# Kernel optimization log

Hardware: AMD Instinct MI355X
Metric: run time of the kernel (lower is better)

Reference implementation:

```python
import jax, jax.numpy as jnp
import numpy as np

N_NODES = 50000
N_REL = 3
N_EDGES = 500000
D_IN, D_HID, D_OUT = 128, 256, 128


def setup_inputs() -> dict:
    key = jax.random.key(0)
    ks = jax.random.split(key, 9)
    def w(k, shape, fan_in):
        return jax.random.normal(k, shape, dtype=jnp.float32) / np.sqrt(fan_in)
    return {
        "x": jax.random.normal(ks[0], (N_NODES, D_IN), dtype=jnp.float32),
        "src": jax.random.randint(ks[1], (N_REL, N_EDGES), 0, N_NODES, dtype=jnp.int32),
        "dst": jax.random.randint(ks[2], (N_REL, N_EDGES), 0, N_NODES, dtype=jnp.int32),
        "w_self1": w(ks[3], (N_REL, D_IN, D_HID), D_IN),
        "w_neigh1": w(ks[4], (N_REL, D_IN, D_HID), D_IN),
        "b1": jnp.zeros((N_REL, D_HID), dtype=jnp.float32),
        "w_self2": w(ks[5], (N_REL, D_HID, D_OUT), D_HID),
        "w_neigh2": w(ks[6], (N_REL, D_HID, D_OUT), D_HID),
        "b2": jnp.zeros((N_REL, D_OUT), dtype=jnp.float32),
    }


def _sage_hetero_layer(x, src, dst, w_self, w_neigh, b):
    """Multi-relation SAGEConv (mean agg); relation outputs summed (HeteroGraphConv default).
    x: [N, din]; src/dst: [R, E]; w_*: [R, din, dout]; b: [R, dout]."""
    n = x.shape[0]

    def per_rel(s, d, ws, wn, bb):
        gathered = jnp.take(x, s, axis=0)                      # [E, din] neighbor gather
        summed = jax.ops.segment_sum(gathered, d, num_segments=n)  # [N, din]
        deg = jax.ops.segment_sum(jnp.ones(s.shape, jnp.float32), d, num_segments=n)
        h_neigh = summed / jnp.maximum(deg, 1.0)[:, None]      # mean, 0 for isolated dst
        return x @ ws + h_neigh @ wn + bb                      # fc_self + fc_neigh + bias

    per_rel_out = jax.vmap(per_rel)(src, dst, w_self, w_neigh, b)  # [R, N, dout]
    return per_rel_out.sum(axis=0)


def reference(x, src, dst, w_self1, w_neigh1, b1, w_self2, w_neigh2, b2):
    h = _sage_hetero_layer(x, src, dst, w_self1, w_neigh1, b1)
    h = jax.nn.relu(h)  # SAGEConv activation in hidden layers
    out = _sage_hetero_layer(h, src, dst, w_self2, w_neigh2, b2)  # last layer: no activation
    return out
```

## Files before the change

kernel.cpp:

```cpp
#include <hip/hip_runtime.h>

#define NN 50000
#define NREL 3
#define NE 500000
#define DIN 128
#define DHID 256
#define DOUT 128

#define NBUK 98
#define CAP 8192
#define EPB 2048
#define NCHK ((NE + EPB - 1) / EPB)
#define PA_BLKS (NREL * NCHK)
#define F2B_BLKS 6250
#define ZROW ((uint)NN << 8)

typedef unsigned int uint;
typedef unsigned short ushort;
typedef __attribute__((ext_vector_type(8))) short bf16x8;
typedef __attribute__((ext_vector_type(4))) float f32x4;

using gptr_t = const __attribute__((address_space(1))) unsigned int*;
using lptr_t = __attribute__((address_space(3))) unsigned int*;

__device__ __forceinline__ ushort f2bf(float f) {
    uint u = __float_as_uint(f);
    uint r = (u + 0x7fffu + ((u >> 16) & 1u)) >> 16;
    return (ushort)r;
}
__device__ __forceinline__ void acc2(float2& a, uint u) {
    a.x += __uint_as_float(u << 16);
    a.y += __uint_as_float(u & 0xffff0000u);
}

__global__ __launch_bounds__(256) void pass_a_prep(
    const int* __restrict__ src, const int* __restrict__ dst,
    int* __restrict__ bcursor, uint* __restrict__ pairs,
    const float* __restrict__ x, ushort* __restrict__ xb,
    const float* __restrict__ ws1, const float* __restrict__ wn1, ushort* __restrict__ Bt1,
    const float* __restrict__ ws2, const float* __restrict__ wn2, ushort* __restrict__ Bt2,
    const float* __restrict__ b1, float* __restrict__ bsum1,
    const float* __restrict__ b2, float* __restrict__ bsum2,
    ushort* __restrict__ agg0, ushort* __restrict__ agg1, ushort* __restrict__ agg2) {
    int blk = blockIdx.x, tid = threadIdx.x;
    if (blk < PA_BLKS) {
        int r = blk / NCHK;
        int chunk = blk % NCHK;
        int e0 = chunk * EPB;
        int nedge = min(EPB, NE - e0);
        const int* S = src + (size_t)r * NE + e0;
        const int* D = dst + (size_t)r * NE + e0;
        __shared__ int cnt[NBUK], base[NBUK], cur[NBUK];
        if (tid < NBUK) { cnt[tid] = 0; cur[tid] = 0; }
        __syncthreads();
        uint pk[8];
        int bk[8];
        bool val[8];
#pragma unroll
        for (int j = 0; j < 8; ++j) {
            int e = j * 256 + tid;
            val[j] = e < nedge;
            int d = val[j] ? D[e] : 0;
            int s = val[j] ? S[e] : 0;
            bk[j] = d >> 9;
            pk[j] = ((uint)s << 9) | (uint)(d & 511);
            if (val[j]) atomicAdd(&cnt[bk[j]], 1);
        }
        __syncthreads();
        if (tid < NBUK) base[tid] = atomicAdd(&bcursor[r * NBUK + tid], cnt[tid]);
        __syncthreads();
#pragma unroll
        for (int j = 0; j < 8; ++j) {
            if (val[j]) {
                int slot = base[bk[j]] + atomicAdd(&cur[bk[j]], 1);
                if (slot < CAP) pairs[(size_t)(r * NBUK + bk[j]) * CAP + slot] = pk[j];
            }
        }
        return;
    }
    blk -= PA_BLKS;
    if (blk < F2B_BLKS) {
        int t = blk * 256 + tid;
        float4 v = *(const float4*)(x + (size_t)t * 4);
        uint2 p;
        p.x = (uint)f2bf(v.x) | ((uint)f2bf(v.y) << 16);
        p.y = (uint)f2bf(v.z) | ((uint)f2bf(v.w) << 16);
        *(uint2*)(xb + (size_t)t * 4) = p;
    } else if (blk < F2B_BLKS + 512) {
        int t = (blk - F2B_BLKS) * 256 + tid;
        int n = t >> 9, k = t & 511;
        int b = k >> 7, kk = k & 127;
        float v;
        if (b == 0)
            v = ws1[kk * 256 + n] + ws1[128 * 256 + kk * 256 + n] + ws1[2 * 128 * 256 + kk * 256 + n];
        else
            v = wn1[(size_t)(b - 1) * 128 * 256 + kk * 256 + n];
        Bt1[t] = f2bf(v);
    } else if (blk < F2B_BLKS + 1024) {
        int t = (blk - F2B_BLKS - 512) * 256 + tid;
        int n = t >> 8, k = t & 255;
        int c = n >> 7, j = n & 127;
        float v;
        if (c == 0)
            v = ws2[k * 128 + j] + ws2[256 * 128 + k * 128 + j] + ws2[2 * 256 * 128 + k * 128 + j];
        else
            v = wn2[(size_t)(c - 1) * 256 * 128 + k * 128 + j];
        Bt2[t] = f2bf(v);
    } else {
        if (tid < DHID) bsum1[tid] = b1[tid] + b1[DHID + tid] + b1[2 * DHID + tid];
        if (tid < DOUT) bsum2[tid] = b2[tid] + b2[DOUT + tid] + b2[2 * DOUT + tid];
        if (tid >= 192 && tid < 256) {
            int b = (tid - 192) >> 4, i = tid & 15;
            ushort* row = (b == 0) ? xb : (b == 1) ? agg0 : (b == 2) ? agg1 : agg2;
            uint4 z = {0u, 0u, 0u, 0u};
            *(uint4*)(row + (size_t)NN * 128 + i * 8) = z;
        }
    }
}

__global__ __launch_bounds__(256) void pass_b(const uint* __restrict__ pairs,
                                              const int* __restrict__ bcnt,
                                              uint* __restrict__ srclist,
                                              int* __restrict__ deg,
                                              int* __restrict__ offs) {
    int blk = blockIdx.x;
    int b = blk % NBUK;
    int r = blk / NBUK;
    int node_base = b * 512;
    int count = min(bcnt[blk], CAP);
    int obase = blk * CAP;
    const uint* pp = pairs + (size_t)blk * CAP;
    __shared__ int hist[512];
    __shared__ int cur[512];
    __shared__ int sc[256];
    int tid = threadIdx.x;
    hist[tid] = 0;
    hist[tid + 256] = 0;
    __syncthreads();
    for (int i = tid; i < count; i += 256) atomicAdd(&hist[pp[i] & 511], 1);
    __syncthreads();
    int v0 = hist[2 * tid], v1 = hist[2 * tid + 1];
    int p0 = (v0 + 7) & ~7;
    int p1 = (v1 + 7) & ~7;
    int s = p0 + p1;
    sc[tid] = s;
    __syncthreads();
    for (int st = 1; st < 256; st <<= 1) {
        int t = (tid >= st) ? sc[tid - st] : 0;
        __syncthreads();
        sc[tid] += t;
        __syncthreads();
    }
    int excl = sc[tid] - s;
    int c0 = obase + excl;
    int c1 = c0 + p0;
    cur[2 * tid] = c0;
    cur[2 * tid + 1] = c1;
    int n0 = node_base + 2 * tid;
    if (n0 < NN)     { deg[r * NN + n0] = v0;     offs[r * NN + n0] = c0; }
    if (n0 + 1 < NN) { deg[r * NN + n0 + 1] = v1; offs[r * NN + n0 + 1] = c1; }
    __syncthreads();
    for (int i = tid; i < count; i += 256) {
        uint p = pp[i];
        int pos = atomicAdd(&cur[p & 511], 1);
        srclist[pos] = (p >> 1) & ~255u;
    }
    __syncthreads();
    for (int i = v0; i < p0; ++i) srclist[c0 + i] = ZROW;
    for (int i = v1; i < p1; ++i) srclist[c1 + i] = ZROW;
}

template <int PHASE>
__global__ __launch_bounds__(256) void gather3(
    const ushort* __restrict__ f0, const ushort* __restrict__ f1,
    const ushort* __restrict__ f2, const int* __restrict__ offs,
    const int* __restrict__ deg, const uint* __restrict__ srclist,
    ushort* __restrict__ ob, float* __restrict__ of) {
    int node = blockIdx.x * 4 + (threadIdx.x >> 6);
    if (node >= NN) return;
    int lane = threadIdx.x & 63;
    int g = lane >> 4;
    uint c16 = (uint)(lane & 15) * 16;
    float2 msum[4];
#pragma unroll
    for (int k = 0; k < 4; ++k) msum[k] = make_float2(0.f, 0.f);

    for (int r = 0; r < NREL; ++r) {
        const char* feat = (const char*)((r == 0) ? f0 : (r == 1) ? f1 : f2);
        int beg = offs[r * NN + node];
        int d = deg[r * NN + node];
        int pd = (d + 7) & ~7;
        float2 ac[4];
#pragma unroll
        for (int k = 0; k < 4; ++k) ac[k] = make_float2(0.f, 0.f);

        for (int i0 = 0; i0 < pd; i0 += 64) {
            uint sid_l = srclist[beg + i0 + lane];
            int lim = pd - i0;
            if (lim > 64) lim = 64;
            for (int j0 = 0; j0 < lim; j0 += 8) {
                uint o1 = __shfl(sid_l, j0 + g) + c16;
                uint o2 = __shfl(sid_l, j0 + 4 + g) + c16;
                uint4 v1 = *(const uint4*)(feat + o1);
                uint4 v2 = *(const uint4*)(feat + o2);
                acc2(ac[0], v1.x); acc2(ac[1], v1.y);
                acc2(ac[2], v1.z); acc2(ac[3], v1.w);
                acc2(ac[0], v2.x); acc2(ac[1], v2.y);
                acc2(ac[2], v2.z); acc2(ac[3], v2.w);
            }
        }
#pragma unroll
        for (int k = 0; k < 4; ++k) {
            ac[k].x += __shfl_xor(ac[k].x, 16);
            ac[k].y += __shfl_xor(ac[k].y, 16);
            ac[k].x += __shfl_xor(ac[k].x, 32);
            ac[k].y += __shfl_xor(ac[k].y, 32);
        }
        float inv = 1.f / fmaxf((float)d, 1.f);
        if (PHASE == 0) {
            if (g == 0) {
                uint4 pk;
                pk.x = (uint)f2bf(ac[0].x * inv) | ((uint)f2bf(ac[0].y * inv) << 16);
                pk.y = (uint)f2bf(ac[1].x * inv) | ((uint)f2bf(ac[1].y * inv) << 16);
                pk.z = (uint)f2bf(ac[2].x * inv) | ((uint)f2bf(ac[2].y * inv) << 16);
                pk.w = (uint)f2bf(ac[3].x * inv) | ((uint)f2bf(ac[3].y * inv) << 16);
                *(uint4*)(ob + (size_t)r * (NN + 1) * DIN + (size_t)node * 128 + (c16 >> 1)) = pk;
            }
        } else {
#pragma unroll
            for (int k = 0; k < 4; ++k) {
                msum[k].x += ac[k].x * inv;
                msum[k].y += ac[k].y * inv;
            }
        }
    }
    if (PHASE == 1 && g == 0) {
        float* po = of + (size_t)node * 128 + (c16 >> 1);
        float4 a = *(float4*)po;
        float4 b = *(float4*)(po + 4);
        a.x += msum[0].x; a.y += msum[0].y; a.z += msum[1].x; a.w += msum[1].y;
        b.x += msum[2].x; b.y += msum[2].y; b.z += msum[3].x; b.w += msum[3].y;
        *(float4*)po = a;
        *(float4*)(po + 4) = b;
    }
}

template <int LAYER>
__global__ __launch_bounds__(512) void gemm_mfma(
    const ushort* __restrict__ A0, const ushort* __restrict__ A1,
    const ushort* __restrict__ A2, const ushort* __restrict__ A3,
    const ushort* __restrict__ Bt, const float* __restrict__ bias,
    ushort* __restrict__ HO, float* __restrict__ CO,
    ushort* __restrict__ Y1, ushort* __restrict__ Y2, ushort* __restrict__ Y3) {
    constexpr int KTOT = (LAYER == 1) ? 512 : 256;
    constexpr int ASTRIDE = (LAYER == 1) ? 128 : 256;
    __shared__ __align__(16) ushort As[128 * 32];
    __shared__ __align__(16) ushort Bs[256 * 32];

    const int tid = threadIdx.x, lane = tid & 63, w = tid >> 6;
    const int wr = w >> 2, wc = w & 3;
    const int bm = blockIdx.x * 128;
    const int bn = blockIdx.y * 256;

    f32x4 acc[4][4];
#pragma unroll
    for (int m = 0; m < 4; ++m)
#pragma unroll
        for (int n = 0; n < 4; ++n) acc[m][n] = (f32x4){0.f, 0.f, 0.f, 0.f};

    const int srow = tid >> 2;
    const int schunk = (tid & 3) * 8;

    for (int k0 = 0; k0 < KTOT; k0 += 32) {
        const ushort* Ab = A0;
        int koff = k0;
        if (LAYER == 1) {
            int b = k0 >> 7;
            Ab = (b == 0) ? A0 : (b == 1) ? A1 : (b == 2) ? A2 : A3;
            koff = k0 & 127;
        }
        {
            const ushort* srcA = Ab + (size_t)(bm + srow) * ASTRIDE + koff + schunk;
            __builtin_amdgcn_global_load_lds((gptr_t)srcA, (lptr_t)(As + w * 512), 16, 0, 0);
        }
#pragma unroll
        for (int i = 0; i < 2; ++i) {
            int row = i * 128 + srow;
            const ushort* srcB = Bt + (size_t)(bn + row) * KTOT + k0 + schunk;
            __builtin_amdgcn_global_load_lds((gptr_t)srcB, (lptr_t)(Bs + i * 4096 + w * 512), 16, 0, 0);
        }
        __syncthreads();

        const int r = lane & 15, g = lane >> 4;
        bf16x8 af[4], bg[4];
#pragma unroll
        for (int m = 0; m < 4; ++m)
            af[m] = *(const bf16x8*)&As[(wr * 64 + m * 16 + r) * 32 + g * 8];
#pragma unroll
        for (int n = 0; n < 4; ++n)
            bg[n] = *(const bf16x8*)&Bs[(wc * 64 + n * 16 + r) * 32 + g * 8];
#pragma unroll
        for (int m = 0; m < 4; ++m)
#pragma unroll
            for (int n = 0; n < 4; ++n)
                acc[m][n] = __builtin_amdgcn_mfma_f32_16x16x32_bf16(af[m], bg[n], acc[m][n], 0, 0, 0);
        __syncthreads();
    }

    const int r = lane & 15, g = lane >> 4;
    if (LAYER == 1) {
#pragma unroll
        for (int m = 0; m < 4; ++m)
#pragma unroll
            for (int v = 0; v < 4; ++v) {
                int gm = bm + wr * 64 + m * 16 + g * 4 + v;
                if (gm >= NN) continue;
#pragma unroll
                for (int n = 0; n < 4; ++n) {
                    int gn = wc * 64 + n * 16 + r;
                    float f = acc[m][n][v] + bias[gn];
                    f = fmaxf(f, 0.f);
                    HO[(size_t)gm * 256 + gn] = f2bf(f);
                }
            }
    } else {
        int buf = (bn >> 7) + (wc >> 1);
        ushort* Y = (buf == 1) ? Y1 : (buf == 2) ? Y2 : Y3;
#pragma unroll
        for (int m = 0; m < 4; ++m)
#pragma unroll
            for (int v = 0; v < 4; ++v) {
                int gm = bm + wr * 64 + m * 16 + g * 4 + v;
                if (gm >= NN) continue;
#pragma unroll
                for (int n = 0; n < 4; ++n) {
                    int col = (wc & 1) * 64 + n * 16 + r;
                    if (buf == 0)
                        CO[(size_t)gm * 128 + col] = acc[m][n][v] + bias[col];
                    else
                        Y[(size_t)gm * 128 + col] = f2bf(acc[m][n][v]);
                }
            }
    }
}

extern "C" void kernel_launch(void* const* d_in, const int* in_sizes, int n_in,
                              void* d_out, int out_size, void* d_ws, size_t ws_size,
                              hipStream_t stream) {
    const float* x        = (const float*)d_in[0];
    const int*   src      = (const int*)d_in[1];
    const int*   dst      = (const int*)d_in[2];
    const float* w_self1  = (const float*)d_in[3];
    const float* w_neigh1 = (const float*)d_in[4];
    const float* b1       = (const float*)d_in[5];
    const float* w_self2  = (const float*)d_in[6];
    const float* w_neigh2 = (const float*)d_in[7];
    const float* b2       = (const float*)d_in[8];
    float* out = (float*)d_out;

    char* ws = (char*)d_ws;
    size_t off = 0;
    auto alloc = [&](size_t bytes) {
        char* p = ws + off;
        off += (bytes + 255) & ~(size_t)255;
        return p;
    };
    const size_t NROW = NN + 1;
    int*    bcursor = (int*)alloc(NREL * NBUK * 4);
    int*    deg     = (int*)alloc(NREL * NN * 4);
    int*    offs    = (int*)alloc(NREL * NN * 4);
    uint*   srclist = (uint*)alloc(((size_t)NREL * NBUK * CAP + 256) * 4);
    float*  bsum1   = (float*)alloc(DHID * 4);
    float*  bsum2   = (float*)alloc(DOUT * 4);
    ushort* Bt1     = (ushort*)alloc((size_t)DHID * 512 * 2);
    ushort* Bt2     = (ushort*)alloc((size_t)512 * DHID * 2);
    ushort* xb      = (ushort*)alloc(NROW * DIN * 2);
    ushort* aggb    = (ushort*)alloc((size_t)NREL * NROW * DIN * 2);
    ushort* Hb      = (ushort*)alloc((size_t)NN * DHID * 2);
    (void)alloc(65536);
    uint* pairs = (uint*)Hb;
    ushort* agg0 = aggb;
    ushort* agg1 = aggb + NROW * DIN;
    ushort* agg2 = aggb + 2 * NROW * DIN;

    hipMemsetAsync(bcursor, 0, NREL * NBUK * 4, stream);
    pass_a_prep<<<PA_BLKS + F2B_BLKS + 1024 + 1, 256, 0, stream>>>(
        src, dst, bcursor, pairs,
        x, xb, w_self1, w_neigh1, Bt1, w_self2, w_neigh2, Bt2,
        b1, bsum1, b2, bsum2, agg0, agg1, agg2);
    pass_b<<<NREL * NBUK, 256, 0, stream>>>(pairs, bcursor, srclist, deg, offs);

    int ggrid = (NN + 3) / 4;

    gather3<0><<<ggrid, 256, 0, stream>>>(xb, xb, xb, offs, deg, srclist, aggb, nullptr);
    {
        dim3 grid((NN + 127) / 128, 1);
        gemm_mfma<1><<<grid, 512, 0, stream>>>(
            xb, agg0, agg1, agg2, Bt1, bsum1, Hb, nullptr, nullptr, nullptr, nullptr);
    }
    {
        dim3 grid((NN + 127) / 128, 2);
        gemm_mfma<2><<<grid, 512, 0, stream>>>(
            Hb, nullptr, nullptr, nullptr, Bt2, bsum2,
            nullptr, out, agg0, agg1, agg2);
    }
    gather3<1><<<ggrid, 256, 0, stream>>>(
        agg0, agg1, agg2, offs, deg, srclist, nullptr, out);
}
```

Before: 240.1 us.

## Interleave three relations' neighbor gathers in one loop and pack deg/offset pairs

The gather kernel now loads all three relations' degree/offset metadata and first 64 source ids up front. It then runs a single merged loop that issues six independent row loads per iteration, one pair per relation, instead of processing relations serially. Relations that run out of neighbors early read a shared zero row, and a tail loop handles degrees above 64. Degree and offset are packed into one int2 array, and accumulation uses 2-wide float vectors so the compiler can emit packed adds. The aim is more memory-level parallelism per wave, at the cost of extra loads of the zero row for unbalanced degrees and higher register pressure.

New measurement: 239.8 us. About the same (-0.1%).

```diff
diff --git a/kernel.cpp b/kernel.cpp
--- a/kernel.cpp
+++ b/kernel.cpp
@@ -19,6 +19,7 @@
 typedef unsigned short ushort;
 typedef __attribute__((ext_vector_type(8))) short bf16x8;
 typedef __attribute__((ext_vector_type(4))) float f32x4;
+typedef __attribute__((ext_vector_type(2))) float f32x2;
 
 using gptr_t = const __attribute__((address_space(1))) unsigned int*;
 using lptr_t = __attribute__((address_space(3))) unsigned int*;
@@ -28,9 +29,14 @@
     uint r = (u + 0x7fffu + ((u >> 16) & 1u)) >> 16;
     return (ushort)r;
 }
-__device__ __forceinline__ void acc2(float2& a, uint u) {
-    a.x += __uint_as_float(u << 16);
-    a.y += __uint_as_float(u & 0xffff0000u);
+__device__ __forceinline__ void acc2(f32x2& a, uint u) {
+    f32x2 t;
+    t.x = __uint_as_float(u << 16);
+    t.y = __uint_as_float(u & 0xffff0000u);
+    a += t;
+}
+__device__ __forceinline__ void acc16(f32x2* a, uint4 v) {
+    acc2(a[0], v.x); acc2(a[1], v.y); acc2(a[2], v.z); acc2(a[3], v.w);
 }
 
 __global__ __launch_bounds__(256) void pass_a_prep(
@@ -121,8 +127,7 @@
 __global__ __launch_bounds__(256) void pass_b(const uint* __restrict__ pairs,
                                               const int* __restrict__ bcnt,
                                               uint* __restrict__ srclist,
-                                              int* __restrict__ deg,
-                                              int* __restrict__ offs) {
+                                              int2* __restrict__ nd) {
     int blk = blockIdx.x;
     int b = blk % NBUK;
     int r = blk / NBUK;
@@ -157,8 +162,8 @@
     cur[2 * tid] = c0;
     cur[2 * tid + 1] = c1;
     int n0 = node_base + 2 * tid;
-    if (n0 < NN)     { deg[r * NN + n0] = v0;     offs[r * NN + n0] = c0; }
-    if (n0 + 1 < NN) { deg[r * NN + n0 + 1] = v1; offs[r * NN + n0 + 1] = c1; }
+    if (n0 < NN)     nd[r * NN + n0]     = make_int2(v0, c0);
+    if (n0 + 1 < NN) nd[r * NN + n0 + 1] = make_int2(v1, c1);
     __syncthreads();
     for (int i = tid; i < count; i += 256) {
         uint p = pp[i];
@@ -173,75 +178,130 @@
 template <int PHASE>
 __global__ __launch_bounds__(256) void gather3(
     const ushort* __restrict__ f0, const ushort* __restrict__ f1,
-    const ushort* __restrict__ f2, const int* __restrict__ offs,
-    const int* __restrict__ deg, const uint* __restrict__ srclist,
+    const ushort* __restrict__ f2, const int2* __restrict__ nd,
+    const uint* __restrict__ srclist,
     ushort* __restrict__ ob, float* __restrict__ of) {
     int node = blockIdx.x * 4 + (threadIdx.x >> 6);
     if (node >= NN) return;
     int lane = threadIdx.x & 63;
     int g = lane >> 4;
     uint c16 = (uint)(lane & 15) * 16;
-    float2 msum[4];
-#pragma unroll
-    for (int k = 0; k < 4; ++k) msum[k] = make_float2(0.f, 0.f);
-
-    for (int r = 0; r < NREL; ++r) {
-        const char* feat = (const char*)((r == 0) ? f0 : (r == 1) ? f1 : f2);
-        int beg = offs[r * NN + node];
-        int d = deg[r * NN + node];
-        int pd = (d + 7) & ~7;
-        float2 ac[4];
-#pragma unroll
-        for (int k = 0; k < 4; ++k) ac[k] = make_float2(0.f, 0.f);
-
-        for (int i0 = 0; i0 < pd; i0 += 64) {
-            uint sid_l = srclist[beg + i0 + lane];
-            int lim = pd - i0;
-            if (lim > 64) lim = 64;
+    const char* fp0 = (const char*)f0;
+    const char* fp1 = (const char*)f1;
+    const char* fp2 = (const char*)f2;
+
+    int2 q0 = nd[node];
+    int2 q1 = nd[NN + node];
+    int2 q2 = nd[2 * NN + node];
+    int d0 = q0.x, d1 = q1.x, d2 = q2.x;
+    int pd0 = (d0 + 7) & ~7, pd1 = (d1 + 7) & ~7, pd2 = (d2 + 7) & ~7;
+    uint sid0 = srclist[q0.y + lane];
+    uint sid1 = srclist[q1.y + lane];
+    uint sid2 = srclist[q2.y + lane];
+
+    f32x2 a0[4], a1[4], a2[4];
+#pragma unroll
+    for (int k = 0; k < 4; ++k) { a0[k] = 0.f; a1[k] = 0.f; a2[k] = 0.f; }
+
+    uint zoff = ZROW + c16;
+    int pmax = max(max(pd0, pd1), pd2);
+    int pm64 = min(pmax, 64);
+    for (int j0 = 0; j0 < pm64; j0 += 8) {
+        uint oA = (j0 < pd0) ? (__shfl(sid0, j0 + g) + c16) : zoff;
+        uint oB = (j0 < pd0) ? (__shfl(sid0, j0 + 4 + g) + c16) : zoff;
+        uint oC = (j0 < pd1) ? (__shfl(sid1, j0 + g) + c16) : zoff;
+        uint oD = (j0 < pd1) ? (__shfl(sid1, j0 + 4 + g) + c16) : zoff;
+        uint oE = (j0 < pd2) ? (__shfl(sid2, j0 + g) + c16) : zoff;
+        uint oF = (j0 < pd2) ? (__shfl(sid2, j0 + 4 + g) + c16) : zoff;
+        uint4 vA = *(const uint4*)(fp0 + oA);
+        uint4 vB = *(const uint4*)(fp0 + oB);
+        uint4 vC = *(const uint4*)(fp1 + oC);
+        uint4 vD = *(const uint4*)(fp1 + oD);
+        uint4 vE = *(const uint4*)(fp2 + oE);
+        uint4 vF = *(const uint4*)(fp2 + oF);
+        acc16(a0, vA); acc16(a0, vB);
+        acc16(a1, vC); acc16(a1, vD);
+        acc16(a2, vE); acc16(a2, vF);
+    }
+    if (pmax > 64) {
+        for (int i0 = 64; i0 < pd0; i0 += 64) {
+            uint sl = srclist[q0.y + i0 + lane];
+            int lim = min(pd0 - i0, 64);
             for (int j0 = 0; j0 < lim; j0 += 8) {
-                uint o1 = __shfl(sid_l, j0 + g) + c16;
-                uint o2 = __shfl(sid_l, j0 + 4 + g) + c16;
-                uint4 v1 = *(const uint4*)(feat + o1);
-                uint4 v2 = *(const uint4*)(feat + o2);
-                acc2(ac[0], v1.x); acc2(ac[1], v1.y);
-                acc2(ac[2], v1.z); acc2(ac[3], v1.w);
-                acc2(ac[0], v2.x); acc2(ac[1], v2.y);
-                acc2(ac[2], v2.z); acc2(ac[3], v2.w);
-            }
-        }
-#pragma unroll
-        for (int k = 0; k < 4; ++k) {
-            ac[k].x += __shfl_xor(ac[k].x, 16);
-            ac[k].y += __shfl_xor(ac[k].y, 16);
-            ac[k].x += __shfl_xor(ac[k].x, 32);
-            ac[k].y += __shfl_xor(ac[k].y, 32);
-        }
-        float inv = 1.f / fmaxf((float)d, 1.f);
-        if (PHASE == 0) {
-            if (g == 0) {
-                uint4 pk;
-                pk.x = (uint)f2bf(ac[0].x * inv) | ((uint)f2bf(ac[0].y * inv) << 16);
-                pk.y = (uint)f2bf(ac[1].x * inv) | ((uint)f2bf(ac[1].y * inv) << 16);
-                pk.z = (uint)f2bf(ac[2].x * inv) | ((uint)f2bf(ac[2].y * inv) << 16);
-                pk.w = (uint)f2bf(ac[3].x * inv) | ((uint)f2bf(ac[3].y * inv) << 16);
-                *(uint4*)(ob + (size_t)r * (NN + 1) * DIN + (size_t)node * 128 + (c16 >> 1)) = pk;
-            }
-        } else {
-#pragma unroll
-            for (int k = 0; k < 4; ++k) {
-                msum[k].x += ac[k].x * inv;
-                msum[k].y += ac[k].y * inv;
-            }
-        }
-    }
-    if (PHASE == 1 && g == 0) {
-        float* po = of + (size_t)node * 128 + (c16 >> 1);
-        float4 a = *(float4*)po;
-        float4 b = *(float4*)(po + 4);
-        a.x += msum[0].x; a.y += msum[0].y; a.z += msum[1].x; a.w += msum[1].y;
-        b.x += msum[2].x; b.y += msum[2].y; b.z += msum[3].x; b.w += msum[3].y;
-        *(float4*)po = a;
-        *(float4*)(po + 4) = b;
+                uint u1 = __shfl(sl, j0 + g) + c16, u2 = __shfl(sl, j0 + 4 + g) + c16;
+                acc16(a0, *(const uint4*)(fp0 + u1));
+                acc16(a0, *(const uint4*)(fp0 + u2));
+            }
+        }
+        for (int i0 = 64; i0 < pd1; i0 += 64) {
+            uint sl = srclist[q1.y + i0 + lane];
+            int lim = min(pd1 - i0, 64);
+            for (int j0 = 0; j0 < lim; j0 += 8) {
+                uint u1 = __shfl(sl, j0 + g) + c16, u2 = __shfl(sl, j0 + 4 + g) + c16;
+                acc16(a1, *(const uint4*)(fp1 + u1));
+                acc16(a1, *(const uint4*)(fp1 + u2));
+            }
+        }
+        for (int i0 = 64; i0 < pd2; i0 += 64) {
+            uint sl = srclist[q2.y + i0 + lane];
+            int lim = min(pd2 - i0, 64);
+            for (int j0 = 0; j0 < lim; j0 += 8) {
+                uint u1 = __shfl(sl, j0 + g) + c16, u2 = __shfl(sl, j0 + 4 + g) + c16;
+                acc16(a2, *(const uint4*)(fp2 + u1));
+                acc16(a2, *(const uint4*)(fp2 + u2));
+            }
+        }
+    }
+
+#pragma unroll
+    for (int k = 0; k < 4; ++k) {
+        a0[k].x += __shfl_xor(a0[k].x, 16); a0[k].y += __shfl_xor(a0[k].y, 16);
+        a0[k].x += __shfl_xor(a0[k].x, 32); a0[k].y += __shfl_xor(a0[k].y, 32);
+        a1[k].x += __shfl_xor(a1[k].x, 16); a1[k].y += __shfl_xor(a1[k].y, 16);
+        a1[k].x += __shfl_xor(a1[k].x, 32); a1[k].y += __shfl_xor(a1[k].y, 32);
+        a2[k].x += __shfl_xor(a2[k].x, 16); a2[k].y += __shfl_xor(a2[k].y, 16);
+        a2[k].x += __shfl_xor(a2[k].x, 32); a2[k].y += __shfl_xor(a2[k].y, 32);
+    }
+    float inv0 = 1.f / fmaxf((float)d0, 1.f);
+    float inv1 = 1.f / fmaxf((float)d1, 1.f);
+    float inv2 = 1.f / fmaxf((float)d2, 1.f);
+    if (PHASE == 0) {
+        if (g == 0) {
+            size_t base = (size_t)node * 128 + (c16 >> 1);
+            size_t rstride = (size_t)(NN + 1) * DIN;
+            uint4 pk;
+            pk.x = (uint)f2bf(a0[0].x * inv0) | ((uint)f2bf(a0[0].y * inv0) << 16);
+            pk.y = (uint)f2bf(a0[1].x * inv0) | ((uint)f2bf(a0[1].y * inv0) << 16);
+            pk.z = (uint)f2bf(a0[2].x * inv0) | ((uint)f2bf(a0[2].y * inv0) << 16);
+            pk.w = (uint)f2bf(a0[3].x * inv0) | ((uint)f2bf(a0[3].y * inv0) << 16);
+            *(uint4*)(ob + base) = pk;
+            pk.x = (uint)f2bf(a1[0].x * inv1) | ((uint)f2bf(a1[0].y * inv1) << 16);
+            pk.y = (uint)f2bf(a1[1].x * inv1) | ((uint)f2bf(a1[1].y * inv1) << 16);
+            pk.z = (uint)f2bf(a1[2].x * inv1) | ((uint)f2bf(a1[2].y * inv1) << 16);
+            pk.w = (uint)f2bf(a1[3].x * inv1) | ((uint)f2bf(a1[3].y * inv1) << 16);
+            *(uint4*)(ob + rstride + base) = pk;
+            pk.x = (uint)f2bf(a2[0].x * inv2) | ((uint)f2bf(a2[0].y * inv2) << 16);
+            pk.y = (uint)f2bf(a2[1].x * inv2) | ((uint)f2bf(a2[1].y * inv2) << 16);
+            pk.z = (uint)f2bf(a2[2].x * inv2) | ((uint)f2bf(a2[2].y * inv2) << 16);
+            pk.w = (uint)f2bf(a2[3].x * inv2) | ((uint)f2bf(a2[3].y * inv2) << 16);
+            *(uint4*)(ob + 2 * rstride + base) = pk;
+        }
+    } else {
+        if (g == 0) {
+            float* po = of + (size_t)node * 128 + (c16 >> 1);
+            float4 a = *(float4*)po;
+            float4 b = *(float4*)(po + 4);
+            a.x += a0[0].x * inv0 + a1[0].x * inv1 + a2[0].x * inv2;
+            a.y += a0[0].y * inv0 + a1[0].y * inv1 + a2[0].y * inv2;
+            a.z += a0[1].x * inv0 + a1[1].x * inv1 + a2[1].x * inv2;
+            a.w += a0[1].y * inv0 + a1[1].y * inv1 + a2[1].y * inv2;
+            b.x += a0[2].x * inv0 + a1[2].x * inv1 + a2[2].x * inv2;
+            b.y += a0[2].y * inv0 + a1[2].y * inv1 + a2[2].y * inv2;
+            b.z += a0[3].x * inv0 + a1[3].x * inv1 + a2[3].x * inv2;
+            b.w += a0[3].y * inv0 + a1[3].y * inv1 + a2[3].y * inv2;
+            *(float4*)po = a;
+            *(float4*)(po + 4) = b;
+        }
     }
 }
 
@@ -367,8 +427,7 @@
     };
     const size_t NROW = NN + 1;
     int*    bcursor = (int*)alloc(NREL * NBUK * 4);
-    int*    deg     = (int*)alloc(NREL * NN * 4);
-    int*    offs    = (int*)alloc(NREL * NN * 4);
+    int2*   nd      = (int2*)alloc((size_t)NREL * NN * 8);
     uint*   srclist = (uint*)alloc(((size_t)NREL * NBUK * CAP + 256) * 4);
     float*  bsum1   = (float*)alloc(DHID * 4);
     float*  bsum2   = (float*)alloc(DOUT * 4);
@@ -388,11 +447,11 @@
         src, dst, bcursor, pairs,
         x, xb, w_self1, w_neigh1, Bt1, w_self2, w_neigh2, Bt2,
         b1, bsum1, b2, bsum2, agg0, agg1, agg2);
-    pass_b<<<NREL * NBUK, 256, 0, stream>>>(pairs, bcursor, srclist, deg, offs);
+    pass_b<<<NREL * NBUK, 256, 0, stream>>>(pairs, bcursor, srclist, nd);
 
     int ggrid = (NN + 3) / 4;
 
-    gather3<0><<<ggrid, 256, 0, stream>>>(xb, xb, xb, offs, deg, srclist, aggb, nullptr);
+    gather3<0><<<ggrid, 256, 0, stream>>>(xb, xb, xb, nd, srclist, aggb, nullptr);
     {
         dim3 grid((NN + 127) / 128, 1);
         gemm_mfma<1><<<grid, 512, 0, stream>>>(
@@ -405,5 +464,5 @@
             nullptr, out, agg0, agg1, agg2);
     }
     gather3<1><<<ggrid, 256, 0, stream>>>(
-        agg0, agg1, agg2, offs, deg, srclist, nullptr, out);
-}
+        agg0, agg1, agg2, nd, srclist, nullptr, out);
+}
```
